# Optimization experiments

Hardware: AMD Instinct MI355X
Metric: run time of the kernel (lower is better)

## Reference

```python
import jax, jax.numpy as jnp
import numpy as np

EPS = 1e-5
PDIM, QKD, DIM = 64, 16, 256
SCALE = QKD ** -0.5


def setup_inputs() -> dict:
    key = jax.random.key(0)
    ks = jax.random.split(key, 13)
    B, H, W = 8, 64, 64
    return {
        "x": jax.random.normal(ks[0], (B, DIM, H, W), jnp.float32),
        "gn_g": jax.random.uniform(ks[1], (PDIM,), jnp.float32, 0.5, 1.5),
        "gn_b": jax.random.normal(ks[2], (PDIM,), jnp.float32) * 0.1,
        "qkv_w": jax.random.normal(ks[3], (2 * QKD + PDIM, PDIM), jnp.float32) * (PDIM ** -0.5),
        "qkv_bn_g": jax.random.uniform(ks[4], (2 * QKD + PDIM,), jnp.float32, 0.5, 1.5),
        "qkv_bn_b": jax.random.normal(ks[5], (2 * QKD + PDIM,), jnp.float32) * 0.1,
        "qkv_rm": jax.random.normal(ks[6], (2 * QKD + PDIM,), jnp.float32) * 0.1,
        "qkv_rv": jax.random.uniform(ks[7], (2 * QKD + PDIM,), jnp.float32, 0.5, 1.5),
        "proj_w": jax.random.normal(ks[8], (DIM, DIM), jnp.float32) * (DIM ** -0.5),
        "proj_bn_g": jax.random.uniform(ks[9], (DIM,), jnp.float32, 0.5, 1.5),
        "proj_bn_b": jax.random.normal(ks[10], (DIM,), jnp.float32) * 0.1,
        "proj_rm": jax.random.normal(ks[11], (DIM,), jnp.float32) * 0.1,
        "proj_rv": jax.random.uniform(ks[12], (DIM,), jnp.float32, 0.5, 1.5),
    }


def _bn(y, g, b, rm, rv):
    # inference BatchNorm over channel axis 1 of [B,C,H,W]
    inv = g / jnp.sqrt(rv + EPS)
    return y * inv[None, :, None, None] + (b - rm * inv)[None, :, None, None]


def reference(x, gn_g, gn_b, qkv_w, qkv_bn_g, qkv_bn_b, qkv_rm, qkv_rv,
              proj_w, proj_bn_g, proj_bn_b, proj_rm, proj_rv):
    B, C, H, W = x.shape
    x1, x2 = x[:, :PDIM], x[:, PDIM:]
    # GroupNorm with 1 group: normalize over (C,H,W) per sample
    mu = jnp.mean(x1, axis=(1, 2, 3), keepdims=True)
    var = jnp.var(x1, axis=(1, 2, 3), keepdims=True)
    x1n = (x1 - mu) / jnp.sqrt(var + EPS)
    x1n = x1n * gn_g[None, :, None, None] + gn_b[None, :, None, None]
    # qkv: 1x1 conv + BN
    qkv = jnp.einsum('bchw,oc->bohw', x1n, qkv_w)
    qkv = _bn(qkv, qkv_bn_g, qkv_bn_b, qkv_rm, qkv_rv)
    q, k, v = qkv[:, :QKD], qkv[:, QKD:2 * QKD], qkv[:, 2 * QKD:]
    N = H * W
    q = q.reshape(B, QKD, N)
    k = k.reshape(B, QKD, N)
    v = v.reshape(B, PDIM, N)
    attn = jnp.einsum('bcn,bcm->bnm', q, k) * SCALE  # [B,N,N]
    attn = jax.nn.softmax(attn, axis=-1)
    x1_attn = jnp.einsum('bcm,bnm->bcn', v, attn).reshape(B, PDIM, H, W)
    xc = jnp.concatenate([x1_attn, x2], axis=1)
    # proj: ReLU -> 1x1 conv -> BN
    y = jnp.einsum('bchw,oc->bohw', jax.nn.relu(xc), proj_w)
    return _bn(y, proj_bn_g, proj_bn_b, proj_rm, proj_rv)
```

## Files before the change

kernel.cpp:

```cpp
#include <hip/hip_runtime.h>
#include <hip/hip_bf16.h>

typedef __bf16 bf16;
typedef __bf16 bf16x4 __attribute__((ext_vector_type(4)));
typedef __bf16 bf16x8 __attribute__((ext_vector_type(8)));
typedef float  f32x16 __attribute__((ext_vector_type(16)));

#define MFMA32 __builtin_amdgcn_mfma_f32_32x32x16_bf16
#define EPSV 1e-5f
#define QSCALE 0.36067376022224085f

__device__ __forceinline__ f32x16 fzero16() {
  f32x16 z;
#pragma unroll
  for (int i = 0; i < 16; ++i) z[i] = 0.f;
  return z;
}

__device__ __forceinline__ void dma16(const void* g, void* s) {
  __builtin_amdgcn_global_load_lds(
      (const __attribute__((address_space(1))) void*)g,
      (__attribute__((address_space(3))) void*)s, 16, 0, 0);
}

__global__ __launch_bounds__(256) void k_stats_partial(const float* __restrict__ x,
                                                       float* __restrict__ part) {
  const int b = blockIdx.x >> 5, k = blockIdx.x & 31;
  const float* p = x + (size_t)b * 256 * 4096 + k * 8192;
  const int t = threadIdx.x;
  float s = 0.f, q = 0.f;
#pragma unroll
  for (int j = 0; j < 8; ++j) {
    float4 v = ((const float4*)p)[t + j * 256];
    s += v.x + v.y + v.z + v.w;
    q += v.x * v.x + v.y * v.y + v.z * v.z + v.w * v.w;
  }
  __shared__ float ls[256], lq[256];
  ls[t] = s; lq[t] = q;
  __syncthreads();
  for (int off = 128; off > 0; off >>= 1) {
    if (t < off) { ls[t] += ls[t + off]; lq[t] += lq[t + off]; }
    __syncthreads();
  }
  if (t == 0) { part[blockIdx.x * 2] = ls[0]; part[blockIdx.x * 2 + 1] = lq[0]; }
}

__global__ __launch_bounds__(256) void k_stats_final(const float* __restrict__ part,
                                                     float* __restrict__ stats) {
  const int t = threadIdx.x, b = t >> 5, k = t & 31;
  float s = part[(b * 32 + k) * 2], q = part[(b * 32 + k) * 2 + 1];
  for (int off = 16; off > 0; off >>= 1) {
    s += __shfl_down(s, off, 32);
    q += __shfl_down(q, off, 32);
  }
  if (k == 0) {
    const float inv_n = 1.f / 262144.f;
    const float mu = s * inv_n;
    const float var = q * inv_n - mu * mu;
    stats[b * 2] = mu;
    stats[b * 2 + 1] = rsqrtf(var + EPSV);
  }
}

__global__ __launch_bounds__(256) void k_qkv(
    const float* __restrict__ x, const float* __restrict__ gn_g, const float* __restrict__ gn_b,
    const float* __restrict__ qkv_w, const float* __restrict__ bn_g, const float* __restrict__ bn_b,
    const float* __restrict__ bn_rm, const float* __restrict__ bn_rv,
    const float* __restrict__ stats,
    bf16* __restrict__ qw, bf16* __restrict__ kw, bf16* __restrict__ vw) {
  const int b = blockIdx.x >> 6, tile = blockIdx.x & 63;
  const int n0 = tile * 64, t = threadIdx.x;
  __shared__ float xn[64][68];
  __shared__ float W[64][96];
  __shared__ float beta_s[96];
  const float mu = stats[b * 2], rstd = stats[b * 2 + 1];
  {
    const int c = t >> 2, f = t & 3;
    const float A = rstd * gn_g[c], B = gn_b[c] - mu * A;
    const float* xr = x + ((size_t)b * 256 + c) * 4096 + n0;
#pragma unroll
    for (int j = 0; j < 4; ++j) {
      float4 v = ((const float4*)xr)[f * 4 + j];
      const int nb = f * 16 + j * 4;
      xn[c][nb + 0] = v.x * A + B; xn[c][nb + 1] = v.y * A + B;
      xn[c][nb + 2] = v.z * A + B; xn[c][nb + 3] = v.w * A + B;
    }
  }
  for (int oc = t; oc < 96 * 8; oc += 256) {
    const int o = oc >> 3, ch = (oc & 7) * 8;
    const float inv = bn_g[o] * rsqrtf(bn_rv[o] + EPSV);
    if (ch == 0) beta_s[o] = bn_b[o] - bn_rm[o] * inv;
    const float* wr = qkv_w + o * 64 + ch;
#pragma unroll
    for (int i = 0; i < 8; ++i) W[ch + i][o] = wr[i] * inv;
  }
  __syncthreads();
  const int o_l = t & 31, ng = t >> 5;
#pragma unroll 1
  for (int p = 0; p < 3; ++p) {
    const int o = p * 32 + o_l;
    float acc[8];
#pragma unroll
    for (int j = 0; j < 8; ++j) acc[j] = 0.f;
    for (int c = 0; c < 64; ++c) {
      const float wv = W[c][o];
      const float* xr = &xn[c][ng * 8];
#pragma unroll
      for (int j = 0; j < 8; ++j) acc[j] += wv * xr[j];
    }
    const float beta = beta_s[o];
    const int nb = n0 + ng * 8;
    if (p == 0) {
      if (o < 16) {
#pragma unroll
        for (int j = 0; j < 8; ++j)
          qw[((size_t)b * 4096 + nb + j) * 16 + o] = (bf16)((acc[j] + beta) * QSCALE);
      } else {
#pragma unroll
        for (int j = 0; j < 8; ++j)
          kw[((size_t)b * 4096 + nb + j) * 16 + (o - 16)] = (bf16)(acc[j] + beta);
      }
    } else {
      const int c = (p - 1) * 32 + o_l;
      const int IT = nb >> 5;
      const int m4 = nb & 31;
      const int f  = ((m4 >> 4) << 1) + (c >> 5);
      const int b3 = (m4 >> 3) & 1;
      char* base = (char*)vw + (size_t)b * 524288 + (size_t)IT * 4096 +
                   f * 1024 + (c & 31) * 16 + b3 * 8;
      bf16x4 pk0, pk1;
#pragma unroll
      for (int i = 0; i < 4; ++i) {
        pk0[i] = (bf16)(acc[i] + beta);
        pk1[i] = (bf16)(acc[4 + i] + beta);
      }
      *(bf16x4*)base = pk0;
      *(bf16x4*)(base + 512) = pk1;
    }
  }
}

__global__ __launch_bounds__(256, 2) void k_attn(
    const bf16* __restrict__ qw, const bf16* __restrict__ kw,
    const bf16* __restrict__ vw, const float* __restrict__ x,
    bf16* __restrict__ xc) {
  __shared__ __align__(16) char smem[40960];
  const int orig = blockIdx.x;
  const int wg = (orig & 7) * 64 + (orig >> 3);
  const int b = wg >> 6, qblk = wg & 63;
  const int t = threadIdx.x;
  const int wid = t >> 6, l = t & 63, ln = l & 31, g = l >> 5;
  const int m0 = wid * 1024;

  const bf16* qb = qw + (size_t)b * 4096 * 16;
  const char* kb = (const char*)(kw + (size_t)b * 4096 * 16);
  const char* vfb = (const char*)vw + (size_t)b * 524288;

  const char* kdma = kb + (size_t)m0 * 32 + (2 * ln + g) * 16;
  const char* vdma = vfb + (size_t)(m0 >> 5) * 4096 + l * 16;
  char* ring = smem + wid * 10240;

  const int nq = qblk * 64 + ln;
  const bf16x8 qf0 = *(const bf16x8*)(qb + (size_t)nq * 16 + g * 8);
  const bf16x8 qf1 = *(const bf16x8*)(qb + (size_t)(nq + 32) * 16 + g * 8);
  asm volatile("" :: "v"(qf0), "v"(qf1));

  f32x16 O00 = fzero16(), O01 = fzero16();
  f32x16 O10 = fzero16(), O11 = fzero16();
  float l0 = 0.f, l1 = 0.f;

#pragma unroll
  for (int pt = 0; pt < 2; ++pt) {
    char* dst = ring + pt * 5120;
    const char* ks = kdma + (size_t)pt * 1024;
    const char* vs = vdma + (size_t)pt * 4096;
    dma16(ks, dst);
    dma16(vs, dst + 1024);
    dma16(vs + 1024, dst + 2048);
    dma16(vs + 2048, dst + 3072);
    dma16(vs + 3072, dst + 4096);
  }

#pragma unroll 1
  for (int it = 0; it < 32; ++it) {
    if (it < 31) { asm volatile("s_waitcnt vmcnt(5)" ::: "memory"); }
    else         { asm volatile("s_waitcnt vmcnt(0)" ::: "memory"); }
    const char* rb = ring + (it & 1) * 5120 + l * 16;
    const uint4 kc = *(const uint4*)rb;
    const uint4 v0 = *(const uint4*)(rb + 1024);
    const uint4 v1 = *(const uint4*)(rb + 2048);
    const uint4 v2 = *(const uint4*)(rb + 3072);
    const uint4 v3 = *(const uint4*)(rb + 4096);
    const bf16x8 kf = __builtin_bit_cast(bf16x8, kc);
    f32x16 S0 = MFMA32(kf, qf0, fzero16(), 0, 0, 0);
    f32x16 S1 = MFMA32(kf, qf1, fzero16(), 0, 0, 0);
    float ts0 = 0.f, ts1 = 0.f;
#pragma unroll
    for (int r = 0; r < 16; ++r) { S0[r] = __builtin_amdgcn_exp2f(S0[r]); ts0 += S0[r]; }
#pragma unroll
    for (int r = 0; r < 16; ++r) { S1[r] = __builtin_amdgcn_exp2f(S1[r]); ts1 += S1[r]; }
    l0 += ts0; l1 += ts1;
    bf16x8 pa0, pa1, pc0, pc1;
#pragma unroll
    for (int r = 0; r < 8; ++r) {
      pa0[r] = (bf16)S0[r]; pa1[r] = (bf16)S0[r + 8];
      pc0[r] = (bf16)S1[r]; pc1[r] = (bf16)S1[r + 8];
    }
    O00 = MFMA32(__builtin_bit_cast(bf16x8, v0), pa0, O00, 0, 0, 0);
    O10 = MFMA32(__builtin_bit_cast(bf16x8, v0), pc0, O10, 0, 0, 0);
    O01 = MFMA32(__builtin_bit_cast(bf16x8, v1), pa0, O01, 0, 0, 0);
    O11 = MFMA32(__builtin_bit_cast(bf16x8, v1), pc0, O11, 0, 0, 0);
    O00 = MFMA32(__builtin_bit_cast(bf16x8, v2), pa1, O00, 0, 0, 0);
    O10 = MFMA32(__builtin_bit_cast(bf16x8, v2), pc1, O10, 0, 0, 0);
    O01 = MFMA32(__builtin_bit_cast(bf16x8, v3), pa1, O01, 0, 0, 0);
    O11 = MFMA32(__builtin_bit_cast(bf16x8, v3), pc1, O11, 0, 0, 0);
    asm volatile("s_waitcnt lgkmcnt(0)" ::: "memory");
    if (it + 2 < 32) {
      char* dst = ring + (it & 1) * 5120;
      const char* ks = kdma + (size_t)(it + 2) * 1024;
      const char* vs = vdma + (size_t)(it + 2) * 4096;
      dma16(ks, dst);
      dma16(vs, dst + 1024);
      dma16(vs + 1024, dst + 2048);
      dma16(vs + 2048, dst + 3072);
      dma16(vs + 3072, dst + 4096);
    }
  }
  l0 += __shfl_xor(l0, 32, 64);
  l1 += __shfl_xor(l1, 32, 64);

  __syncthreads();

  {
    const int msk = 2 * (ln & 7);
#pragma unroll
    for (int hq = 0; hq < 2; ++hq) {
      char* orow = smem + (wid * 2 + hq) * 4096 + ln * 128;
#pragma unroll
      for (int hc = 0; hc < 2; ++hc) {
        const f32x16& O = hq ? (hc ? O11 : O10) : (hc ? O01 : O00);
#pragma unroll
        for (int j = 0; j < 4; ++j) {
          bf16x4 e;
#pragma unroll
          for (int i = 0; i < 4; ++i) e[i] = (bf16)O[4 * j + i];
          const int chunk = hc * 8 + 2 * j + g;
          *(bf16x4*)(orow + ((chunk ^ msk) << 3)) = e;
        }
      }
      if (g == 0) *(float*)(smem + 32768 + (wid * 2 + hq) * 128 + ln * 4) = hq ? l1 : l0;
    }
  }
  __syncthreads();

  {
    const int n = t >> 3, k8 = t & 7;
    const int off = ((2 * k8) ^ (2 * (n & 7))) << 3;
#pragma unroll
    for (int hq = 0; hq < 2; ++hq) {
      float L = 0.f;
      float acc[8];
#pragma unroll
      for (int e = 0; e < 8; ++e) acc[e] = 0.f;
#pragma unroll
      for (int kr_ = 0; kr_ < 4; ++kr_) {
        const int s = kr_ * 2 + hq;
        L += *(const float*)(smem + 32768 + s * 128 + n * 4);
        const bf16x8 v = *(const bf16x8*)(smem + s * 4096 + n * 128 + off);
#pragma unroll
        for (int e = 0; e < 8; ++e) acc[e] += (float)v[e];
      }
      const float rL = 1.0f / L;
      bf16x8 o8;
#pragma unroll
      for (int e = 0; e < 8; ++e) o8[e] = (bf16)fmaxf(acc[e] * rL, 0.f);
      *(bf16x8*)(xc + ((size_t)b * 4096 + qblk * 64 + hq * 32 + n) * 256 + k8 * 8) = o8;
    }
  }
  __syncthreads();

  {
    unsigned* tile_u = (unsigned*)smem;
    const float* xb = x + ((size_t)b * 256 + 64) * 4096 + qblk * 64;
#pragma unroll
    for (int i = 0; i < 6; ++i) {
      const int idx = i * 256 + t;
      const int cp = idx >> 4, f = idx & 15;
      const float4 a = *(const float4*)(xb + (size_t)(2 * cp) * 4096 + f * 4);
      const float4 c4 = *(const float4*)(xb + (size_t)(2 * cp + 1) * 4096 + f * 4);
      const float av[4] = {a.x, a.y, a.z, a.w};
      const float cv[4] = {c4.x, c4.y, c4.z, c4.w};
#pragma unroll
      for (int e = 0; e < 4; ++e) {
        const unsigned u =
            (unsigned)__builtin_bit_cast(unsigned short, (bf16)fmaxf(av[e], 0.f)) |
            ((unsigned)__builtin_bit_cast(unsigned short, (bf16)fmaxf(cv[e], 0.f)) << 16);
        tile_u[(f * 4 + e) * 97 + cp] = u;
      }
    }
    __syncthreads();
#pragma unroll
    for (int i = 0; i < 6; ++i) {
      const int idx = i * 256 + t;
      const int n = idx / 24, q = idx % 24;
      const uint4 d = *(const uint4*)&tile_u[n * 97 + q * 4];
      *(uint4*)(xc + ((size_t)b * 4096 + qblk * 64 + n) * 256 + 64 + q * 8) = d;
    }
  }
}

__global__ __launch_bounds__(256, 2) void k_proj(
    const bf16* __restrict__ xc, const float* __restrict__ pw,
    const float* __restrict__ bn_g, const float* __restrict__ bn_b,
    const float* __restrict__ bn_rm, const float* __restrict__ bn_rv,
    float* __restrict__ out) {
  const int orig = blockIdx.x;
  const int wg = (orig & 7) * 64 + (orig >> 3);
  const int b = wg >> 6, rem = wg & 63, nt = rem >> 1, oh = rem & 1;
  const int n0 = nt * 128, o0 = oh * 128;
  const int t = threadIdx.x, w = t >> 6, l = t & 63, ln = l & 31, g = l >> 5;

  __shared__ __align__(16) bf16 pws[128 * 256];
  __shared__ float beta_s[128];

  {
    const int o = t >> 1, half = t & 1;
    const float inv = bn_g[o0 + o] * rsqrtf(bn_rv[o0 + o] + EPSV);
    if (half == 0) beta_s[o] = bn_b[o0 + o] - bn_rm[o0 + o] * inv;
    const float* wr = pw + (size_t)(o0 + o) * 256 + half * 128;
    const int s_hh = (o & 15) * 8;
#pragma unroll
    for (int j = 0; j < 16; ++j) {
      const float4 a = ((const float4*)wr)[j * 2];
      const float4 c4 = ((const float4*)wr)[j * 2 + 1];
      bf16x8 v8;
      v8[0] = (bf16)(a.x * inv);  v8[1] = (bf16)(a.y * inv);
      v8[2] = (bf16)(a.z * inv);  v8[3] = (bf16)(a.w * inv);
      v8[4] = (bf16)(c4.x * inv); v8[5] = (bf16)(c4.y * inv);
      v8[6] = (bf16)(c4.z * inv); v8[7] = (bf16)(c4.w * inv);
      *(bf16x8*)&pws[o * 256 + ((half * 128 + j * 8) ^ s_hh)] = v8;
    }
  }
  __syncthreads();

  const bf16* xrow = xc + ((size_t)b * 4096 + n0 + w * 32 + ln) * 256;
  const int sw = (ln & 15) * 8;
  f32x16 acc0 = fzero16(), acc1 = fzero16(), acc2 = fzero16(), acc3 = fzero16();
#pragma unroll 4
  for (int ck = 0; ck < 256; ck += 16) {
    const bf16x8 bfrag = *(const bf16x8*)(xrow + ck + g * 8);
    const int cidx = (ck + g * 8) ^ sw;
    const bf16x8 a0 = *(const bf16x8*)&pws[(ln) * 256 + cidx];
    const bf16x8 a1 = *(const bf16x8*)&pws[(32 + ln) * 256 + cidx];
    const bf16x8 a2 = *(const bf16x8*)&pws[(64 + ln) * 256 + cidx];
    const bf16x8 a3 = *(const bf16x8*)&pws[(96 + ln) * 256 + cidx];
    acc0 = MFMA32(a0, bfrag, acc0, 0, 0, 0);
    acc1 = MFMA32(a1, bfrag, acc1, 0, 0, 0);
    acc2 = MFMA32(a2, bfrag, acc2, 0, 0, 0);
    acc3 = MFMA32(a3, bfrag, acc3, 0, 0, 0);
  }
  const int ncol = n0 + w * 32 + ln;
  float* ob = out + (size_t)b * 256 * 4096 + ncol;
#pragma unroll
  for (int og = 0; og < 4; ++og) {
    const f32x16& A = og == 0 ? acc0 : og == 1 ? acc1 : og == 2 ? acc2 : acc3;
#pragma unroll
    for (int r = 0; r < 16; ++r) {
      const int o_loc = og * 32 + (r & 3) + 8 * (r >> 2) + 4 * g;
      ob[(size_t)(o0 + o_loc) * 4096] = A[r] + beta_s[o_loc];
    }
  }
}

extern "C" void kernel_launch(void* const* d_in, const int* in_sizes, int n_in,
                              void* d_out, int out_size, void* d_ws, size_t ws_size,
                              hipStream_t stream) {
  (void)in_sizes; (void)n_in; (void)out_size; (void)ws_size;
  const float* x        = (const float*)d_in[0];
  const float* gn_g     = (const float*)d_in[1];
  const float* gn_b     = (const float*)d_in[2];
  const float* qkv_w    = (const float*)d_in[3];
  const float* qkv_bn_g = (const float*)d_in[4];
  const float* qkv_bn_b = (const float*)d_in[5];
  const float* qkv_rm   = (const float*)d_in[6];
  const float* qkv_rv   = (const float*)d_in[7];
  const float* proj_w   = (const float*)d_in[8];
  const float* proj_bn_g = (const float*)d_in[9];
  const float* proj_bn_b = (const float*)d_in[10];
  const float* proj_rm  = (const float*)d_in[11];
  const float* proj_rv  = (const float*)d_in[12];

  char* ws = (char*)d_ws;
  float* part  = (float*)ws;
  float* stats = (float*)(ws + 4096);
  bf16* qw = (bf16*)(ws + 8192);
  bf16* kw = (bf16*)(ws + 8192 + (1u << 20));
  bf16* vw = (bf16*)(ws + 8192 + (2u << 20));
  bf16* xc = (bf16*)(ws + 8192 + (6u << 20));

  k_stats_partial<<<256, 256, 0, stream>>>(x, part);
  k_stats_final<<<1, 256, 0, stream>>>(part, stats);
  k_qkv<<<512, 256, 0, stream>>>(x, gn_g, gn_b, qkv_w, qkv_bn_g, qkv_bn_b,
                                 qkv_rm, qkv_rv, stats, qw, kw, vw);
  k_attn<<<512, 256, 0, stream>>>(qw, kw, vw, x, xc);
  k_proj<<<512, 256, 0, stream>>>(xc, proj_w, proj_bn_g, proj_bn_b,
                                  proj_rm, proj_rv, (float*)d_out);
}
```

Baseline: 87.48 us.

## Deepen K/V DMA ring to three stages and issue prefetch before compute

Expands the per-wave LDS ring from two to three K/V tile slots and issues the next tile's global-to-LDS loads right after the current tile is read into registers, rather than after the MFMAs. The vmcnt waits are adjusted so that two tiles stay in flight. The row-sum of the exponentials is also changed from a serial chain to a tree reduction. Shared memory per block grows to 60 KB, which may limit how many blocks fit per CU alongside the launch bound of 2.

```diff
diff --git a/kernel.cpp b/kernel.cpp
--- a/kernel.cpp
+++ b/kernel.cpp
@@ -144,7 +144,7 @@
     const bf16* __restrict__ qw, const bf16* __restrict__ kw,
     const bf16* __restrict__ vw, const float* __restrict__ x,
     bf16* __restrict__ xc) {
-  __shared__ __align__(16) char smem[40960];
+  __shared__ __align__(16) char smem[61440];
   const int orig = blockIdx.x;
   const int wg = (orig & 7) * 64 + (orig >> 3);
   const int b = wg >> 6, qblk = wg & 63;
@@ -158,7 +158,7 @@
 
   const char* kdma = kb + (size_t)m0 * 32 + (2 * ln + g) * 16;
   const char* vdma = vfb + (size_t)(m0 >> 5) * 4096 + l * 16;
-  char* ring = smem + wid * 10240;
+  char* ring = smem + wid * 15360;
 
   const int nq = qblk * 64 + ln;
   const bf16x8 qf0 = *(const bf16x8*)(qb + (size_t)nq * 16 + g * 8);
@@ -169,37 +169,55 @@
   f32x16 O10 = fzero16(), O11 = fzero16();
   float l0 = 0.f, l1 = 0.f;
 
-#pragma unroll
-  for (int pt = 0; pt < 2; ++pt) {
-    char* dst = ring + pt * 5120;
-    const char* ks = kdma + (size_t)pt * 1024;
-    const char* vs = vdma + (size_t)pt * 4096;
-    dma16(ks, dst);
-    dma16(vs, dst + 1024);
-    dma16(vs + 1024, dst + 2048);
-    dma16(vs + 2048, dst + 3072);
-    dma16(vs + 3072, dst + 4096);
-  }
-
+#define ISSUE_TILE(TI, SLOT)                                  \
+  do {                                                        \
+    char* dst = ring + (SLOT) * 5120;                         \
+    const char* ks = kdma + (size_t)(TI) * 1024;              \
+    const char* vs = vdma + (size_t)(TI) * 4096;              \
+    dma16(ks, dst);                                           \
+    dma16(vs, dst + 1024);                                    \
+    dma16(vs + 1024, dst + 2048);                             \
+    dma16(vs + 2048, dst + 3072);                             \
+    dma16(vs + 3072, dst + 4096);                             \
+  } while (0)
+
+  ISSUE_TILE(0, 0);
+  ISSUE_TILE(1, 1);
+  ISSUE_TILE(2, 2);
+
+  int slot = 0;
 #pragma unroll 1
   for (int it = 0; it < 32; ++it) {
-    if (it < 31) { asm volatile("s_waitcnt vmcnt(5)" ::: "memory"); }
-    else         { asm volatile("s_waitcnt vmcnt(0)" ::: "memory"); }
-    const char* rb = ring + (it & 1) * 5120 + l * 16;
+    const int rem = 31 - it;
+    if (rem >= 2)      { asm volatile("s_waitcnt vmcnt(10)" ::: "memory"); }
+    else if (rem == 1) { asm volatile("s_waitcnt vmcnt(5)"  ::: "memory"); }
+    else               { asm volatile("s_waitcnt vmcnt(0)"  ::: "memory"); }
+    const char* rb = ring + slot * 5120 + l * 16;
     const uint4 kc = *(const uint4*)rb;
     const uint4 v0 = *(const uint4*)(rb + 1024);
     const uint4 v1 = *(const uint4*)(rb + 2048);
     const uint4 v2 = *(const uint4*)(rb + 3072);
     const uint4 v3 = *(const uint4*)(rb + 4096);
+    asm volatile("s_waitcnt lgkmcnt(0)" ::: "memory");
+    if (it + 3 < 32) ISSUE_TILE(it + 3, slot);
     const bf16x8 kf = __builtin_bit_cast(bf16x8, kc);
     f32x16 S0 = MFMA32(kf, qf0, fzero16(), 0, 0, 0);
     f32x16 S1 = MFMA32(kf, qf1, fzero16(), 0, 0, 0);
-    float ts0 = 0.f, ts1 = 0.f;
-#pragma unroll
-    for (int r = 0; r < 16; ++r) { S0[r] = __builtin_amdgcn_exp2f(S0[r]); ts0 += S0[r]; }
-#pragma unroll
-    for (int r = 0; r < 16; ++r) { S1[r] = __builtin_amdgcn_exp2f(S1[r]); ts1 += S1[r]; }
-    l0 += ts0; l1 += ts1;
+#pragma unroll
+    for (int r = 0; r < 16; ++r) S0[r] = __builtin_amdgcn_exp2f(S0[r]);
+#pragma unroll
+    for (int r = 0; r < 16; ++r) S1[r] = __builtin_amdgcn_exp2f(S1[r]);
+    {
+      float a[8], c[8];
+#pragma unroll
+      for (int r = 0; r < 8; ++r) { a[r] = S0[2 * r] + S0[2 * r + 1];
+                                    c[r] = S1[2 * r] + S1[2 * r + 1]; }
+#pragma unroll
+      for (int r = 0; r < 4; ++r) { a[r] = a[2 * r] + a[2 * r + 1];
+                                    c[r] = c[2 * r] + c[2 * r + 1]; }
+      l0 += (a[0] + a[1]) + (a[2] + a[3]);
+      l1 += (c[0] + c[1]) + (c[2] + c[3]);
+    }
     bf16x8 pa0, pa1, pc0, pc1;
 #pragma unroll
     for (int r = 0; r < 8; ++r) {
@@ -214,18 +232,9 @@
     O10 = MFMA32(__builtin_bit_cast(bf16x8, v2), pc1, O10, 0, 0, 0);
     O01 = MFMA32(__builtin_bit_cast(bf16x8, v3), pa1, O01, 0, 0, 0);
     O11 = MFMA32(__builtin_bit_cast(bf16x8, v3), pc1, O11, 0, 0, 0);
-    asm volatile("s_waitcnt lgkmcnt(0)" ::: "memory");
-    if (it + 2 < 32) {
-      char* dst = ring + (it & 1) * 5120;
-      const char* ks = kdma + (size_t)(it + 2) * 1024;
-      const char* vs = vdma + (size_t)(it + 2) * 4096;
-      dma16(ks, dst);
-      dma16(vs, dst + 1024);
-      dma16(vs + 1024, dst + 2048);
-      dma16(vs + 2048, dst + 3072);
-      dma16(vs + 3072, dst + 4096);
-    }
-  }
+    slot = (slot == 2) ? 0 : slot + 1;
+  }
+#undef ISSUE_TILE
   l0 += __shfl_xor(l0, 32, 64);
   l1 += __shfl_xor(l1, 32, 64);
 
```

Measured after the change: 85.97 us. Within noise of the previous version (-1.7%).
